# Kernel optimization log

Measured on AMD Instinct MI355X. Metric: run time of the kernel, lower is better.

The kernel has to match this reference:

```python
import jax, jax.numpy as jnp
import numpy as np

L = 64
N = L * L
WIDTH = 2
LOG2L = int(np.log2(L))


def _build_perm(L):
    # fold ordering: site (0,0) first, then quad-tree levels coarse->fine,
    # three sublattices per level, row-major within each slice (matches torch reshape)
    perm = [0]
    for i in range(LOG2L - 1, -1, -1):
        s, p = 2 ** i, 2 ** (i + 1)
        for rows, cols in [(np.arange(s, L, p), np.arange(s, L, p)),
                           (np.arange(s, L, p), np.arange(0, L, p)),
                           (np.arange(0, L, p), np.arange(s, L, p))]:
            perm.extend((rows[:, None] * L + cols[None, :]).ravel())
    return np.asarray(perm, dtype=np.int64)


def _build_levels():
    lvl = np.zeros(N, dtype=np.int64)
    k = 1
    for i in range(LOG2L):
        base = 4 ** i
        for idx, length in [(base, base), (2 * base, base), (3 * base, base)]:
            lvl[idx:idx + length] = k
            k += 1
    return lvl


def _build_mask(lvl, in_ch, out_ch, exclusive):
    m = (lvl[None, :] < lvl[:, None]) if exclusive else (lvl[None, :] <= lvl[:, None])
    return np.tile(m.astype(np.float32), (out_ch, in_ch))  # [out_ch*N, in_ch*N]


PERM = _build_perm(L)
INV = np.empty(N, dtype=np.int64)
INV[PERM] = np.arange(N)
_LVL = _build_levels()
M0 = jnp.asarray(_build_mask(_LVL, 1, WIDTH, True))      # [WIDTH*N, N]
M1 = jnp.asarray(_build_mask(_LVL, WIDTH, WIDTH, False))  # [WIDTH*N, WIDTH*N]
M2 = jnp.asarray(_build_mask(_LVL, WIDTH, 1, False))      # [N, WIDTH*N]
XHAT_MASK = jnp.ones(N, jnp.float32).at[0].set(0.0)
XHAT_BIAS = jnp.zeros(N, jnp.float32).at[0].set(0.5)


def _prelu(x, a):
    return jnp.maximum(x, 0.0) + a * jnp.minimum(x, 0.0)


def setup_inputs() -> dict:
    key = jax.random.key(0)
    ks = jax.random.split(key, 9)
    B = 128
    x = jnp.sign(jax.random.normal(ks[0], (B, L, L), jnp.float32))  # +/-1 spins
    sc = 0.02
    return {
        'x': x,
        'W0': jax.random.normal(ks[1], (WIDTH * N, N), jnp.float32) * sc,
        'b0': jax.random.normal(ks[2], (WIDTH * N,), jnp.float32) * sc,
        'a1': jnp.full((WIDTH * N,), 0.5, jnp.float32),
        'W1': jax.random.normal(ks[3], (WIDTH * N, WIDTH * N), jnp.float32) * sc,
        'b1': jax.random.normal(ks[4], (WIDTH * N,), jnp.float32) * sc,
        'a2': jnp.full((WIDTH * N,), 0.5, jnp.float32),
        'W2': jax.random.normal(ks[5], (N, WIDTH * N), jnp.float32) * sc,
        'b2': jax.random.normal(ks[6], (N,), jnp.float32) * sc,
    }


def reference(x, W0, b0, a1, W1, b1, a2, W2, b2):
    B = x.shape[0]
    xf = x.reshape(B, N)[:, PERM]                 # fold via precomputed gather
    h = xf @ (W0 * M0).T + b0                     # exclusive masked linear 1->WIDTH
    h = _prelu(h, a1)
    h = h @ (W1 * M1).T + b1                      # masked linear WIDTH->WIDTH
    h = _prelu(h, a2)
    h = h @ (W2 * M2).T + b2                      # masked linear WIDTH->1
    x_hat = jax.nn.sigmoid(h)
    x_hat = x_hat * XHAT_MASK + XHAT_BIAS         # bias & not z2 path
    return x_hat[:, INV].reshape(B, L, L)         # unfold via inverse permutation
```

## Files before the change

### kernel.cpp

```cpp
#include <hip/hip_runtime.h>
#include <hip/hip_bf16.h>
#include <cstddef>
#include <cstdint>

#define NN 4096
#define BB 128

using short8 = __attribute__((ext_vector_type(8))) short;
using f32x4  = __attribute__((ext_vector_type(4))) float;

__device__ __forceinline__ void klims(int r, int& S, int& E) {
    if (r == 0) { S = 0; E = 1; return; }
    int j = (31 - __clz(r)) >> 1;
    int g = r >> (2 * j);
    S = g << (2 * j);
    E = (g + 1) << (2 * j);
}

__device__ __forceinline__ int perm_site(int n) {
    if (n == 0) return 0;
    int j = (31 - __clz(n)) >> 1;
    int g = n >> (2 * j);
    int o = n - (g << (2 * j));
    int side = 1 << j;
    int rr = o >> j, cc = o & (side - 1);
    int i = 5 - j;
    int s = 1 << i, p = 1 << (i + 1);
    int r, c;
    if (g == 1)      { r = s + rr * p; c = s + cc * p; }
    else if (g == 2) { r = s + rr * p; c = cc * p;     }
    else             { r = rr * p;     c = s + cc * p; }
    return r * 64 + c;
}

__device__ __forceinline__ int inv_site(int s) {
    if (s == 0) return 0;
    int r = s >> 6, c = s & 63;
    int ir = r ? __builtin_ctz(r) : 6;
    int ic = c ? __builtin_ctz(c) : 6;
    int i = ir < ic ? ir : ic;
    int j = 5 - i;
    int rb = (r >> i) & 1, cb = (c >> i) & 1;
    int g = rb ? (cb ? 1 : 2) : 3;
    return (g << (2 * j)) + ((r >> (i + 1)) << j) + (c >> (i + 1));
}

__device__ __forceinline__ size_t fidx(int k, int b) {
    return (size_t)(((k >> 5) * 8 + (b >> 4)) * 512 + ((k >> 2) & 3) * 128 +
                    (b & 15) * 8 + ((k >> 4) & 1) * 4 + (k & 3));
}

__device__ __forceinline__ unsigned short f2bf(float f) {
    __hip_bfloat16 h = __float2bfloat16(f);
    return __builtin_bit_cast(unsigned short, h);
}

__device__ __forceinline__ void gload_lds16(const void* g, void* l) {
    __builtin_amdgcn_global_load_lds(
        (const __attribute__((address_space(1))) unsigned int*)g,
        (__attribute__((address_space(3))) unsigned int*)l, 16, 0, 0);
}

__device__ __forceinline__ int tile_nt(int M, int tile, int nseg, int excl) {
    int r_top = (M - 1 - tile * 128) & (NN - 1);
    int S, E;
    klims(r_top, S, E);
    int kmax = excl ? S : E;
    return nseg * ((kmax + 63) >> 6);
}

__global__ void fold_k(const float* __restrict__ x, unsigned short* __restrict__ xf) {
    int gid = blockIdx.x * 256 + threadIdx.x;
    int b = gid >> 12, s = gid & 4095;
    float v = x[gid];
    int n = inv_site(s);
    xf[fidx(n, b)] = f2bf(v);
}

template <bool EXCL>
__global__ __launch_bounds__(512, 2) void made_gemm11(
        const unsigned short* __restrict__ A, const float* __restrict__ W,
        float* __restrict__ partial, int M, int Ktot, int nseg, int CH) {
    __shared__ __align__(16) char lds[32768];

    int b = (int)blockIdx.x, tile = 0, base = 0, nt = 0;
    for (;;) {
        nt = tile_nt(M, tile, nseg, EXCL ? 1 : 0);
        int cnt = (nt + CH - 1) / CH;
        if (b < base + cnt) break;
        base += cnt;
        ++tile;
    }
    const int nkt = nt / nseg;
    const int t0 = (b - base) * CH;
    const int t1 = (t0 + CH < nt) ? t0 + CH : nt;

    const int tid  = threadIdx.x;
    const int wid  = tid >> 6;
    const int lane = tid & 63;
    const int r0   = M - 128 - tile * 128;
    const int rw0  = r0 + wid * 16;
    const int rch  = rw0 & (NN - 1);
    const int row  = lane & 15;
    const int kq   = lane >> 4;

    int S, E;
    klims(rch + row, S, E);
    const int kl = EXCL ? S : E;
    klims(rch, S, E);
    const int wkmin = EXCL ? S : E;

    f32x4 acc[8] = {};
    const float* wrow = W + (size_t)(rw0 + row) * Ktot + kq * 4;
    const char* Ab = (const char*)A;

    float4 wbA[4], wbB[4];

#define ISSUE_W(T, WB)                                                        \
    {                                                                         \
        int sg_ = (nseg == 2 && (T) >= nkt) ? 1 : 0;                          \
        const float* wp_ = wrow + sg_ * NN + (((T) - sg_ * nkt) << 6);        \
        WB[0] = *(const float4*)(wp_);                                        \
        WB[1] = *(const float4*)(wp_ + 16);                                   \
        WB[2] = *(const float4*)(wp_ + 32);                                   \
        WB[3] = *(const float4*)(wp_ + 48);                                   \
    }

#define STAGE_A(T, BUF)                                                       \
    {                                                                         \
        int sg_ = (nseg == 2 && (T) >= nkt) ? 1 : 0;                          \
        int kb_ = ((T) - sg_ * nkt) << 6;                                     \
        const char* src_ = Ab + (size_t)(sg_ * NN + kb_) * 256 +              \
                           wid * 2048 + lane * 16;                            \
        char* dst_ = lds + (BUF) * 16384 + wid * 2048;                        \
        gload_lds16(src_, dst_);                                              \
        gload_lds16(src_ + 1024, dst_ + 1024);                                \
    }

#define COMPUTE_L(T, BUF, WB)                                                 \
    {                                                                         \
        int kb_ = (((T) >= nkt && nseg == 2) ? (T) - nkt : (T)) << 6;         \
        float wv_[16];                                                        \
        _Pragma("unroll")                                                     \
        for (int i_ = 0; i_ < 4; ++i_) {                                      \
            wv_[4 * i_ + 0] = WB[i_].x;                                       \
            wv_[4 * i_ + 1] = WB[i_].y;                                       \
            wv_[4 * i_ + 2] = WB[i_].z;                                       \
            wv_[4 * i_ + 3] = WB[i_].w;                                       \
        }                                                                     \
        if (kb_ + 64 > wkmin) {                                               \
            int k0_ = kb_ + kq * 4;                                           \
            _Pragma("unroll")                                                 \
            for (int i_ = 0; i_ < 4; ++i_) {                                  \
                _Pragma("unroll")                                             \
                for (int j_ = 0; j_ < 4; ++j_)                                \
                    if (k0_ + i_ * 16 + j_ >= kl) wv_[4 * i_ + j_] = 0.0f;    \
            }                                                                 \
        }                                                                     \
        short8 wf0_, wf1_;                                                    \
        _Pragma("unroll")                                                     \
        for (int e_ = 0; e_ < 8; ++e_) {                                      \
            wf0_[e_] = (short)f2bf(wv_[e_]);                                  \
            wf1_[e_] = (short)f2bf(wv_[8 + e_]);                              \
        }                                                                     \
        const char* ab_ = lds + (BUF) * 16384 + lane * 16;                    \
        _Pragma("unroll")                                                     \
        for (int q_ = 0; q_ < 8; ++q_) {                                      \
            short8 a0_ = *(const short8*)(ab_ + q_ * 1024);                   \
            short8 a1_ = *(const short8*)(ab_ + 8192 + q_ * 1024);            \
            acc[q_] = __builtin_amdgcn_mfma_f32_16x16x32_bf16(                \
                wf0_, a0_, acc[q_], 0, 0, 0);                                 \
            acc[q_] = __builtin_amdgcn_mfma_f32_16x16x32_bf16(                \
                wf1_, a1_, acc[q_], 0, 0, 0);                                 \
        }                                                                     \
    }

    {
        int t = t0, buf = 0;
        STAGE_A(t, 0);
        ISSUE_W(t, wbA);
        while (true) {
            __syncthreads();
            bool pre = (t + 1 < t1);
            if (pre) { STAGE_A(t + 1, buf ^ 1); ISSUE_W(t + 1, wbB); }
            COMPUTE_L(t, buf, wbA);
            if (!pre) break;
            ++t; buf ^= 1;
            __syncthreads();
            pre = (t + 1 < t1);
            if (pre) { STAGE_A(t + 1, buf ^ 1); ISSUE_W(t + 1, wbA); }
            COMPUTE_L(t, buf, wbB);
            if (!pre) break;
            ++t; buf ^= 1;
        }
    }
#undef ISSUE_W
#undef STAGE_A
#undef COMPUTE_L

    float* pc = partial + (size_t)blockIdx.x * 16384 + (wid * 16 + kq * 4) * 128 + row;
#pragma unroll
    for (int q = 0; q < 8; ++q)
#pragma unroll
        for (int i = 0; i < 4; ++i)
            pc[(size_t)i * 128 + q * 16] = acc[q][i];
}

__global__ void reduce01_k(const float* __restrict__ p, const float* __restrict__ bias,
                           const float* __restrict__ alpha, unsigned short* __restrict__ h,
                           int M, int nseg, int excl, int CH) {
    int gid = blockIdx.x * 256 + threadIdx.x;
    int m0 = (gid >> 7) << 2;
    int b  = gid & 127;
    int tile_m = (M - 128 - (m0 & ~127)) >> 7;
    int basep = 0, cntm = 0;
    for (int tt = 0; tt <= tile_m; ++tt) {
        int nt = tile_nt(M, tt, nseg, excl);
        int cnt = (nt + CH - 1) / CH;
        if (tt == tile_m) cntm = cnt;
        else basep += cnt;
    }
    const float* ps = p + (size_t)basep * 16384 + (m0 & 127) * 128 + b;
    f32x4 v = {};
    for (int s = 0; s < cntm; ++s) {
        v[0] += ps[0];
        v[1] += ps[128];
        v[2] += ps[256];
        v[3] += ps[384];
        ps += 16384;
    }
    ushort4 st;
    float t;
    t = v[0] + bias[m0 + 0]; t = fmaxf(t, 0.f) + alpha[m0 + 0] * fminf(t, 0.f); st.x = f2bf(t);
    t = v[1] + bias[m0 + 1]; t = fmaxf(t, 0.f) + alpha[m0 + 1] * fminf(t, 0.f); st.y = f2bf(t);
    t = v[2] + bias[m0 + 2]; t = fmaxf(t, 0.f) + alpha[m0 + 2] * fminf(t, 0.f); st.z = f2bf(t);
    t = v[3] + bias[m0 + 3]; t = fmaxf(t, 0.f) + alpha[m0 + 3] * fminf(t, 0.f); st.w = f2bf(t);
    *(ushort4*)&h[fidx(m0, b)] = st;
}

__global__ void reduce2_k(const float* __restrict__ p, const float* __restrict__ b2,
                          float* __restrict__ out, int CH) {
    int gid = blockIdx.x * 256 + threadIdx.x;
    int n = gid >> 7;
    int b = gid & 127;
    int tile_m = (NN - 128 - (n & ~127)) >> 7;
    int basep = 0, cntm = 0;
    for (int tt = 0; tt <= tile_m; ++tt) {
        int nt = tile_nt(NN, tt, 2, 0);
        int cnt = (nt + CH - 1) / CH;
        if (tt == tile_m) cntm = cnt;
        else basep += cnt;
    }
    const float* ps = p + (size_t)basep * 16384 + (n & 127) * 128 + b;
    float v = 0.0f;
    for (int s = 0; s < cntm; ++s) { v += *ps; ps += 16384; }
    v += b2[n];
    float sg = 1.0f / (1.0f + __expf(-v));
    if (n == 0) sg = 0.5f;
    out[(size_t)b * NN + perm_site(n)] = sg;
}

static inline void h_klims(int r, int& S, int& E) {
    if (r == 0) { S = 0; E = 1; return; }
    int j = (31 - __builtin_clz((unsigned)r)) >> 1;
    int g = r >> (2 * j);
    S = g << (2 * j);
    E = (g + 1) << (2 * j);
}

static inline int grid_for(int M, int nseg, int excl, int CH) {
    int nb = 0;
    for (int tile = 0; tile < M / 128; ++tile) {
        int r_top = (M - 1 - tile * 128) & (NN - 1);
        int S, E;
        h_klims(r_top, S, E);
        int kmax = excl ? S : E;
        int nt = nseg * ((kmax + 63) >> 6);
        nb += (nt + CH - 1) / CH;
    }
    return nb;
}

extern "C" void kernel_launch(void* const* d_in, const int* in_sizes, int n_in,
                              void* d_out, int out_size, void* d_ws, size_t ws_size,
                              hipStream_t stream) {
    const float* x  = (const float*)d_in[0];
    const float* W0 = (const float*)d_in[1];
    const float* b0 = (const float*)d_in[2];
    const float* a1 = (const float*)d_in[3];
    const float* W1 = (const float*)d_in[4];
    const float* b1 = (const float*)d_in[5];
    const float* a2 = (const float*)d_in[6];
    const float* W2 = (const float*)d_in[7];
    const float* b2 = (const float*)d_in[8];

    char* ws = (char*)d_ws;
    unsigned short* xf = (unsigned short*)ws;
    unsigned short* h0 = (unsigned short*)(ws + (1 << 20));
    unsigned short* h1 = (unsigned short*)(ws + (3 << 20));
    float*          pp = (float*)(ws + (5 << 20));

    int CH = 128;
    int g0 = 0, g1 = 0, g2 = 0;
    const int cands[5] = {8, 16, 32, 64, 128};
    for (int ci = 0; ci < 5; ++ci) {
        int c = cands[ci];
        int a = grid_for(2 * NN, 1, 1, c);
        int bA = grid_for(2 * NN, 2, 0, c);
        int cC = grid_for(NN, 2, 0, c);
        int gmax = a > bA ? a : bA;
        if (cC > gmax) gmax = cC;
        size_t need = (size_t)(5 << 20) + (size_t)gmax * 65536;
        if (need <= ws_size || ci == 4) {
            CH = c; g0 = a; g1 = bA; g2 = cC;
            break;
        }
    }

    fold_k<<<2048, 256, 0, stream>>>(x, xf);

    made_gemm11<true><<<g0, 512, 0, stream>>>(xf, W0, pp, 2 * NN, NN, 1, CH);
    reduce01_k<<<1024, 256, 0, stream>>>(pp, b0, a1, h0, 2 * NN, 1, 1, CH);

    made_gemm11<false><<<g1, 512, 0, stream>>>(h0, W1, pp, 2 * NN, 2 * NN, 2, CH);
    reduce01_k<<<1024, 256, 0, stream>>>(pp, b1, a2, h1, 2 * NN, 2, 0, CH);

    made_gemm11<false><<<g2, 512, 0, stream>>>(h1, W2, pp, NN, 2 * NN, 2, CH);
    reduce2_k<<<2048, 256, 0, stream>>>(pp, b2, (float*)d_out, CH);
}
```

Baseline: 156.7 us.

## Swizzle workgroups across XCDs and use per-layer split-K chunk sizes

Adds an XCD-aware remapping of block indices so that consecutive logical workgroups, which share the same row tile and weight/activation data, land on the same XCD and its L2. It also replaces the old search over a single chunk size with fixed per-layer chunk sizes (8, 16, 8), which gives finer split-K grids and falls back to 128 only if the workspace is too small. Smaller chunks mean more partial buffers and more reduction work, traded for better load balance and occupancy across CUs.

```diff
diff --git a/kernel.cpp b/kernel.cpp
--- a/kernel.cpp
+++ b/kernel.cpp
@@ -69,6 +69,13 @@
     return nseg * ((kmax + 63) >> 6);
 }
 
+__device__ __forceinline__ int xcd_swz(int p, int nwg) {
+    int xcd = p & 7, i = p >> 3;
+    int q = nwg >> 3, r = nwg & 7;
+    int base = (xcd < r) ? xcd * (q + 1) : r * (q + 1) + (xcd - r) * q;
+    return base + i;
+}
+
 __global__ void fold_k(const float* __restrict__ x, unsigned short* __restrict__ xf) {
     int gid = blockIdx.x * 256 + threadIdx.x;
     int b = gid >> 12, s = gid & 4095;
@@ -78,12 +85,13 @@
 }
 
 template <bool EXCL>
-__global__ __launch_bounds__(512, 2) void made_gemm11(
+__global__ __launch_bounds__(512, 2) void made_gemm17(
         const unsigned short* __restrict__ A, const float* __restrict__ W,
-        float* __restrict__ partial, int M, int Ktot, int nseg, int CH) {
+        float* __restrict__ partial, int M, int Ktot, int nseg, int CH, int nwg) {
     __shared__ __align__(16) char lds[32768];
 
-    int b = (int)blockIdx.x, tile = 0, base = 0, nt = 0;
+    const int wg = xcd_swz((int)blockIdx.x, nwg);
+    int b = wg, tile = 0, base = 0, nt = 0;
     for (;;) {
         nt = tile_nt(M, tile, nseg, EXCL ? 1 : 0);
         int cnt = (nt + CH - 1) / CH;
@@ -198,7 +206,7 @@
 #undef STAGE_A
 #undef COMPUTE_L
 
-    float* pc = partial + (size_t)blockIdx.x * 16384 + (wid * 16 + kq * 4) * 128 + row;
+    float* pc = partial + (size_t)wg * 16384 + (wid * 16 + kq * 4) * 128 + row;
 #pragma unroll
     for (int q = 0; q < 8; ++q)
 #pragma unroll
@@ -300,31 +308,27 @@
     unsigned short* h1 = (unsigned short*)(ws + (3 << 20));
     float*          pp = (float*)(ws + (5 << 20));
 
-    int CH = 128;
-    int g0 = 0, g1 = 0, g2 = 0;
-    const int cands[5] = {8, 16, 32, 64, 128};
-    for (int ci = 0; ci < 5; ++ci) {
-        int c = cands[ci];
-        int a = grid_for(2 * NN, 1, 1, c);
-        int bA = grid_for(2 * NN, 2, 0, c);
-        int cC = grid_for(NN, 2, 0, c);
-        int gmax = a > bA ? a : bA;
-        if (cC > gmax) gmax = cC;
-        size_t need = (size_t)(5 << 20) + (size_t)gmax * 65536;
-        if (need <= ws_size || ci == 4) {
-            CH = c; g0 = a; g1 = bA; g2 = cC;
-            break;
-        }
+    int CH0 = 8, CH1 = 16, CH2 = 8;
+    int g0 = grid_for(2 * NN, 1, 1, CH0);
+    int g1 = grid_for(2 * NN, 2, 0, CH1);
+    int g2 = grid_for(NN, 2, 0, CH2);
+    int gmax = g0 > g1 ? g0 : g1;
+    if (g2 > gmax) gmax = g2;
+    if ((size_t)(5 << 20) + (size_t)gmax * 65536 > ws_size) {
+        CH0 = CH1 = CH2 = 128;
+        g0 = grid_for(2 * NN, 1, 1, CH0);
+        g1 = grid_for(2 * NN, 2, 0, CH1);
+        g2 = grid_for(NN, 2, 0, CH2);
     }
 
     fold_k<<<2048, 256, 0, stream>>>(x, xf);
 
-    made_gemm11<true><<<g0, 512, 0, stream>>>(xf, W0, pp, 2 * NN, NN, 1, CH);
-    reduce01_k<<<1024, 256, 0, stream>>>(pp, b0, a1, h0, 2 * NN, 1, 1, CH);
-
-    made_gemm11<false><<<g1, 512, 0, stream>>>(h0, W1, pp, 2 * NN, 2 * NN, 2, CH);
-    reduce01_k<<<1024, 256, 0, stream>>>(pp, b1, a2, h1, 2 * NN, 2, 0, CH);
-
-    made_gemm11<false><<<g2, 512, 0, stream>>>(h1, W2, pp, NN, 2 * NN, 2, CH);
-    reduce2_k<<<2048, 256, 0, stream>>>(pp, b2, (float*)d_out, CH);
-}
+    made_gemm17<true><<<g0, 512, 0, stream>>>(xf, W0, pp, 2 * NN, NN, 1, CH0, g0);
+    reduce01_k<<<1024, 256, 0, stream>>>(pp, b0, a1, h0, 2 * NN, 1, 1, CH0);
+
+    made_gemm17<false><<<g1, 512, 0, stream>>>(h0, W1, pp, 2 * NN, 2 * NN, 2, CH1, g1);
+    reduce01_k<<<1024, 256, 0, stream>>>(pp, b1, a2, h1, 2 * NN, 2, 0, CH1);
+
+    made_gemm17<false><<<g2, 512, 0, stream>>>(h1, W2, pp, NN, 2 * NN, 2, CH2, g2);
+    reduce2_k<<<2048, 256, 0, stream>>>(pp, b2, (float*)d_out, CH2);
+}
```

Result: slower. 163.0 us (+4.0%).
